# Kernel optimization log

Measured on AMD Instinct MI355X. Metric: run time of the kernel, lower is better.

The kernel has to match this reference:

```python
import jax, jax.numpy as jnp
import numpy as np

N_HEAD = 16
TOPK = 2


def _forward(x, noise, Wk, Wv, Wq, Wo, Wg, Wn):
    B, T, C = x.shape
    E = Wg.shape[1]
    H = N_HEAD
    D = C // H
    x2 = x.reshape(-1, C)  # [N, C], N = B*T
    # noisy gating: logits + randn * softplus(noise_proj)
    gate_logits = x2 @ Wg + noise * jax.nn.softplus(x2 @ Wn)  # [N, E]
    w, sel = jax.lax.top_k(gate_logits, TOPK)                 # [N, K]
    w = jax.nn.softmax(w.astype(jnp.float32), axis=1).astype(x.dtype)
    # shared keys/values across experts
    k = (x @ Wk).reshape(B, T, H, D)
    v = (x @ Wv).reshape(B, T, H, D)
    # per-expert queries for all tokens, gathered per selected expert below
    q_all = jnp.einsum('btc,eco->bteo', x, Wq)  # [B, T, E, C]
    causal = jnp.tril(jnp.ones((T, T), dtype=bool))  # key j visible to query t iff j <= t
    scale = 1.0 / np.sqrt(D).astype(np.float32)
    sel_bt = sel.reshape(B, T, TOPK)
    w_bt = w.reshape(B, T, TOPK)
    out = jnp.zeros_like(x)
    for s in range(TOPK):  # small fixed loop over top-k slots
        e = sel_bt[:, :, s]  # [B, T] expert id per token
        q = jnp.take_along_axis(q_all, e[:, :, None, None], axis=2)[:, :, 0, :]  # [B, T, C]
        qh = q.reshape(B, T, H, D)
        scores = jnp.einsum('bthd,bjhd->bhtj', qh, k) * scale  # [B, H, T, T]
        scores = jnp.where(causal[None, None], scores, -jnp.inf)
        p = jax.nn.softmax(scores, axis=-1)
        attn = jnp.einsum('bhtj,bjhd->bthd', p, v).reshape(B, T, C)
        o_all = jnp.einsum('btc,eco->bteo', attn, Wo)  # [B, T, E, C]
        o = jnp.take_along_axis(o_all, e[:, :, None, None], axis=2)[:, :, 0, :]
        out = out + w_bt[:, :, s:s + 1] * o
    return out


def setup_inputs() -> dict:
    key = jax.random.key(0)
    ks = jax.random.split(key, 8)
    B, T, C, E = 4, 1024, 1024, 8
    s = 0.02
    x = jax.random.normal(ks[0], (B, T, C), jnp.float32)
    noise = jax.random.normal(ks[1], (B * T, E), jnp.float32)
    Wk = jax.random.normal(ks[2], (C, C), jnp.float32) * s
    Wv = jax.random.normal(ks[3], (C, C), jnp.float32) * s
    Wq = jax.random.normal(ks[4], (E, C, C), jnp.float32) * s
    Wo = jax.random.normal(ks[5], (E, C, C), jnp.float32) * s
    Wg = jax.random.normal(ks[6], (C, E), jnp.float32) * s
    Wn = jax.random.normal(ks[7], (C, E), jnp.float32) * s
    return {'x': x, 'noise': noise, 'Wk': Wk, 'Wv': Wv, 'Wq': Wq, 'Wo': Wo, 'Wg': Wg, 'Wn': Wn}


def reference(x, noise, Wk, Wv, Wq, Wo, Wg, Wn):
    return _forward(x, noise, Wk, Wv, Wq, Wo, Wg, Wn)
```

## Files before the change

kernel.cpp:

```cpp
#include <hip/hip_runtime.h>
#include <hip/hip_bf16.h>

#define TSEQ   1024
#define NC     1024
#define MBT    4096
#define NEXP   8
#define NHEAD  16
#define DHEAD  64
#define PERM_CAP 10240
#define MAXTILES 96

typedef __attribute__((ext_vector_type(8))) short bf16x8;
typedef __attribute__((ext_vector_type(4))) float f32x4;

static __device__ __forceinline__ unsigned short f2bf(float x){
    union { __hip_bfloat16 h; unsigned short u; } v;
    v.h = __float2bfloat16(x);
    return v.u;
}

__global__ __launch_bounds__(64)
void gate_kernel(const float* __restrict__ x, const float* __restrict__ noise,
                 const float* __restrict__ Wg, const float* __restrict__ Wn,
                 int* __restrict__ epair, float* __restrict__ wpair){
    int t = blockIdx.x;
    int lane = threadIdx.x;
    float ag[8] = {0,0,0,0,0,0,0,0};
    float an[8] = {0,0,0,0,0,0,0,0};
    const float* xr = x + (size_t)t * NC;
    for (int c = lane; c < NC; c += 64){
        float xv = xr[c];
        #pragma unroll
        for (int j = 0; j < 8; j++){
            ag[j] = fmaf(xv, Wg[c*8 + j], ag[j]);
            an[j] = fmaf(xv, Wn[c*8 + j], an[j]);
        }
    }
    #pragma unroll
    for (int j = 0; j < 8; j++){
        #pragma unroll
        for (int o = 32; o >= 1; o >>= 1){
            ag[j] += __shfl_xor(ag[j], o, 64);
            an[j] += __shfl_xor(an[j], o, 64);
        }
    }
    if (lane == 0){
        float lg[8];
        #pragma unroll
        for (int j = 0; j < 8; j++){
            float z = an[j];
            float sp = (z > 20.f) ? z : log1pf(expf(z));
            lg[j] = ag[j] + noise[(size_t)t*8 + j] * sp;
        }
        int i0 = 0; float v0 = lg[0];
        #pragma unroll
        for (int j = 1; j < 8; j++) if (lg[j] > v0){ v0 = lg[j]; i0 = j; }
        int i1 = -1; float v1 = -3.4e38f;
        #pragma unroll
        for (int j = 0; j < 8; j++) if (j != i0 && lg[j] > v1){ v1 = lg[j]; i1 = j; }
        float e1 = expf(v1 - v0);
        float w0 = 1.f / (1.f + e1);
        epair[2*t]   = i0;
        epair[2*t+1] = i1;
        wpair[2*t]   = w0;
        wpair[2*t+1] = e1 * w0;
    }
}

__global__ void transpose_cvt(const float* __restrict__ W, unsigned short* __restrict__ Wt){
    __shared__ float t[32][33];
    size_t base = (size_t)blockIdx.z * NC * NC;
    int k0 = blockIdx.x * 32, n0 = blockIdx.y * 32;
    int tx = threadIdx.x, ty = threadIdx.y;
    #pragma unroll
    for (int i = 0; i < 4; i++)
        t[ty + i*8][tx] = W[base + (size_t)(k0 + ty + i*8)*NC + n0 + tx];
    __syncthreads();
    #pragma unroll
    for (int i = 0; i < 4; i++)
        Wt[base + (size_t)(n0 + ty + i*8)*NC + k0 + tx] = f2bf(t[tx][ty + i*8]);
}

__global__ void cvt_x(const float* __restrict__ x, unsigned short* __restrict__ xb){
    int idx = blockIdx.x * blockDim.x + threadIdx.x;
    float4 v = ((const float4*)x)[idx];
    ushort4 o;
    o.x = f2bf(v.x); o.y = f2bf(v.y); o.z = f2bf(v.z); o.w = f2bf(v.w);
    ((ushort4*)xb)[idx] = o;
}

__global__ void transpose_v(const unsigned short* __restrict__ kvb, unsigned short* __restrict__ vbT){
    __shared__ unsigned short sh[32][33];
    int b = blockIdx.z;
    int c0 = blockIdx.x * 32, t0 = blockIdx.y * 32;
    int tx = threadIdx.x, ty = threadIdx.y;
    #pragma unroll
    for (int i = 0; i < 4; i++)
        sh[ty + i*8][tx] = kvb[((size_t)(b*TSEQ + t0 + ty + i*8))*2048 + 1024 + c0 + tx];
    __syncthreads();
    #pragma unroll
    for (int i = 0; i < 4; i++){
        int c = c0 + ty + i*8;
        vbT[((size_t)(b*NC + c))*TSEQ + t0 + tx] = sh[tx][ty + i*8];
    }
}

__global__ void group_build(const int* __restrict__ epair, int* __restrict__ cursor,
                            int* __restrict__ tile_g, int* __restrict__ tile_pos,
                            int* __restrict__ ntiles, int* __restrict__ perm){
    __shared__ int cnt[16];
    int tid = threadIdx.x;
    if (tid < 16) cnt[tid] = 0;
    __syncthreads();
    for (int p = tid; p < 2*MBT; p += 256){
        int g = ((p & 1) << 3) | epair[p];
        atomicAdd(&cnt[g], 1);
    }
    for (int i = tid; i < PERM_CAP; i += 256) perm[i] = -1;
    __syncthreads();
    if (tid == 0){
        int off = 0, tt = 0;
        for (int g = 0; g < 16; g++){
            int c = cnt[g];
            cursor[g] = off;
            int nt = (c + 127) >> 7;
            for (int i = 0; i < nt; i++){ tile_g[tt] = g; tile_pos[tt] = off + i*128; tt++; }
            off += nt << 7;
        }
        ntiles[0] = tt;
    }
}

__global__ void fill_perm(const int* __restrict__ epair, int* __restrict__ cursor,
                          int* __restrict__ perm){
    int p = blockIdx.x * blockDim.x + threadIdx.x;
    if (p < 2*MBT){
        int g = ((p & 1) << 3) | epair[p];
        int pos = atomicAdd(&cursor[g], 1);
        perm[pos] = p;
    }
}

template<int MODE>
__global__ __launch_bounds__(256)
void gemm_k(const unsigned short* __restrict__ A,
            const unsigned short* __restrict__ Bt,
            void* __restrict__ Cout,
            const int* __restrict__ perm,
            const int* __restrict__ tile_g,
            const int* __restrict__ tile_pos,
            const int* __restrict__ ntiles,
            const float* __restrict__ wpair,
            int nout){
    int ntile = blockIdx.x;
    int slot  = blockIdx.y;
    int tpos = 0;
    const unsigned short* bt = Bt;
    if (MODE != 0){
        if (slot >= ntiles[0]) return;
        int g = tile_g[slot];
        bt = Bt + (size_t)(g & 7) * NC * NC;
        tpos = tile_pos[slot];
    }
    __shared__ __align__(16) unsigned short As[128][72];
    __shared__ __align__(16) unsigned short Bs[128][72];
    int tid = threadIdx.x;
    int lane = tid & 63, wv = tid >> 6;
    int wr = wv >> 1, wc = wv & 1;
    int quad = lane >> 4, l15 = lane & 15;

    int r0 = tid >> 3;
    int c8 = (tid & 7) * 8;
    const unsigned short* ap[4];
    const unsigned short* bp[4];
    #pragma unroll
    for (int i = 0; i < 4; i++){
        int row = r0 + i*32;
        if (MODE == 0){
            ap[i] = A + (size_t)(slot*128 + row) * NC + c8;
        } else {
            int p = perm[tpos + row];
            if (p >= 0){
                if (MODE == 1) ap[i] = A + (size_t)(p >> 1) * NC + c8;
                else           ap[i] = A + (size_t)(p & 1) * MBT * NC + (size_t)(p >> 1) * NC + c8;
            } else ap[i] = nullptr;
        }
        bp[i] = bt + (size_t)(ntile*128 + row) * NC + c8;
    }

    f32x4 acc[4][4];
    #pragma unroll
    for (int i = 0; i < 4; i++)
        #pragma unroll
        for (int j = 0; j < 4; j++) acc[i][j] = (f32x4){0.f,0.f,0.f,0.f};

    for (int kk = 0; kk < NC; kk += 64){
        #pragma unroll
        for (int i = 0; i < 4; i++){
            int row = r0 + i*32;
            uint4 av = ap[i] ? *(const uint4*)(ap[i] + kk) : make_uint4(0,0,0,0);
            uint4 bv = *(const uint4*)(bp[i] + kk);
            *(uint4*)&As[row][c8] = av;
            *(uint4*)&Bs[row][c8] = bv;
        }
        __syncthreads();
        #pragma unroll
        for (int kh = 0; kh < 2; kh++){
            bf16x8 af[4], bfr[4];
            #pragma unroll
            for (int mi = 0; mi < 4; mi++) af[mi]  = *(const bf16x8*)&As[wr*64 + mi*16 + l15][kh*32 + quad*8];
            #pragma unroll
            for (int ni = 0; ni < 4; ni++) bfr[ni] = *(const bf16x8*)&Bs[wc*64 + ni*16 + l15][kh*32 + quad*8];
            #pragma unroll
            for (int mi = 0; mi < 4; mi++)
                #pragma unroll
                for (int ni = 0; ni < 4; ni++)
                    acc[mi][ni] = __builtin_amdgcn_mfma_f32_16x16x32_bf16(af[mi], bfr[ni], acc[mi][ni], 0, 0, 0);
        }
        __syncthreads();
    }

    int colbase = ntile*128 + wc*64 + l15;
    #pragma unroll
    for (int mi = 0; mi < 4; mi++){
        #pragma unroll
        for (int r = 0; r < 4; r++){
            int m = wr*64 + mi*16 + quad*4 + r;
            if (MODE == 0){
                unsigned short* co = (unsigned short*)Cout + (size_t)(slot*128 + m) * nout + colbase;
                #pragma unroll
                for (int ni = 0; ni < 4; ni++) co[ni*16] = f2bf(acc[mi][ni][r]);
            } else {
                int p = perm[tpos + m];
                if (p >= 0){
                    if (MODE == 1){
                        unsigned short* co = (unsigned short*)Cout + (size_t)p * NC + colbase;
                        #pragma unroll
                        for (int ni = 0; ni < 4; ni++) co[ni*16] = f2bf(0.125f * acc[mi][ni][r]);
                    } else {
                        float w = wpair[p];
                        float* co = (float*)Cout + (size_t)(p & 1) * MBT * NC + (size_t)(p >> 1) * NC + colbase;
                        #pragma unroll
                        for (int ni = 0; ni < 4; ni++) co[ni*16] = w * acc[mi][ni][r];
                    }
                }
            }
        }
    }
}

__global__ void combine(const float* __restrict__ os, float* __restrict__ out){
    size_t i = ((size_t)blockIdx.x * 256 + threadIdx.x) * 4;
    float4 a = *(const float4*)(os + i);
    float4 b = *(const float4*)(os + (size_t)MBT*NC + i);
    float4 r; r.x = a.x+b.x; r.y = a.y+b.y; r.z = a.z+b.z; r.w = a.w+b.w;
    *(float4*)(out + i) = r;
}

__global__ __launch_bounds__(256)
void attn_k(const unsigned short* __restrict__ qsel, const unsigned short* __restrict__ kvb,
            const unsigned short* __restrict__ vbT, unsigned short* __restrict__ attnb){
    int b = blockIdx.y >> 4, h = blockIdx.y & 15;
    int s = blockIdx.z;
    int tid = threadIdx.x, lane = tid & 63, wv = tid >> 6;
    int quad = lane >> 4, l15 = lane & 15;

    __shared__ __align__(16) unsigned short ksh[64][72];
    __shared__ __align__(16) unsigned short vsh[64][72];
    __shared__ __align__(16) unsigned short pwork[4][32][72];

    #pragma unroll
    for (int half = 0; half < 2; half++){
        int qb = half ? (7 - blockIdx.x) : blockIdx.x;
        int qbase = qb*128 + wv*32;
        int ig[2] = { qbase + l15, qbase + 16 + l15 };

        bf16x8 qf[2][2];
        #pragma unroll
        for (int isub = 0; isub < 2; isub++){
            const unsigned short* qrow = qsel + (((size_t)(b*TSEQ + qbase + isub*16 + l15))*2 + s)*NC + h*DHEAD;
            qf[isub][0] = *(const bf16x8*)(qrow + quad*8);
            qf[isub][1] = *(const bf16x8*)(qrow + 32 + quad*8);
        }

        float mrun[2] = {-1e30f, -1e30f}, lrun[2] = {0.f, 0.f};
        f32x4 oacc[4][2];
        #pragma unroll
        for (int d = 0; d < 4; d++)
            #pragma unroll
            for (int i = 0; i < 2; i++) oacc[d][i] = (f32x4){0.f,0.f,0.f,0.f};

        int njt = qb*2 + 2;
        for (int jt = 0; jt < njt; jt++){
            #pragma unroll
            for (int it = 0; it < 2; it++){
                int idx = it*256 + tid;
                int r = idx >> 3, cc = (idx & 7) * 8;
                *(uint4*)&ksh[r][cc] = *(const uint4*)(kvb + ((size_t)(b*TSEQ + jt*64 + r))*2048 + h*DHEAD + cc);
                *(uint4*)&vsh[r][cc] = *(const uint4*)(vbT + ((size_t)(b*NC + h*DHEAD + r))*TSEQ + jt*64 + cc);
            }
            __syncthreads();

            if (jt*64 <= qbase + 31){
                f32x4 sac[4][2];
                #pragma unroll
                for (int jsub = 0; jsub < 4; jsub++){
                    bf16x8 kf0 = *(const bf16x8*)&ksh[jsub*16 + l15][quad*8];
                    bf16x8 kf1 = *(const bf16x8*)&ksh[jsub*16 + l15][32 + quad*8];
                    #pragma unroll
                    for (int isub = 0; isub < 2; isub++){
                        f32x4 z = (f32x4){0.f,0.f,0.f,0.f};
                        z = __builtin_amdgcn_mfma_f32_16x16x32_bf16(kf0, qf[isub][0], z, 0, 0, 0);
                        z = __builtin_amdgcn_mfma_f32_16x16x32_bf16(kf1, qf[isub][1], z, 0, 0, 0);
                        sac[jsub][isub] = z;
                    }
                }
                bool need_mask = (jt*64 + 63 > qbase);
                float sv[2][16];
                #pragma unroll
                for (int jsub = 0; jsub < 4; jsub++){
                    #pragma unroll
                    for (int r = 0; r < 4; r++){
                        int j = jt*64 + jsub*16 + quad*4 + r;
                        #pragma unroll
                        for (int isub = 0; isub < 2; isub++){
                            float v = sac[jsub][isub][r];
                            if (need_mask && j > ig[isub]) v = -1e30f;
                            sv[isub][jsub*4 + r] = v;
                        }
                    }
                }
                #pragma unroll
                for (int isub = 0; isub < 2; isub++){
                    float tm = sv[isub][0];
                    #pragma unroll
                    for (int k = 1; k < 16; k++) tm = fmaxf(tm, sv[isub][k]);
                    tm = fmaxf(tm, __shfl_xor(tm, 16, 64));
                    tm = fmaxf(tm, __shfl_xor(tm, 32, 64));
                    float mn = fmaxf(mrun[isub], tm);
                    float alpha = __expf(mrun[isub] - mn);
                    float rs = 0.f;
                    #pragma unroll
                    for (int k = 0; k < 16; k++){
                        float p = __expf(sv[isub][k] - mn);
                        sv[isub][k] = p; rs += p;
                    }
                    rs += __shfl_xor(rs, 16, 64);
                    rs += __shfl_xor(rs, 32, 64);
                    lrun[isub] = lrun[isub]*alpha + rs; mrun[isub] = mn;
                    #pragma unroll
                    for (int d = 0; d < 4; d++) oacc[d][isub] = oacc[d][isub] * alpha;
                    #pragma unroll
                    for (int jsub = 0; jsub < 4; jsub++){
                        ushort4 pk;
                        pk.x = f2bf(sv[isub][jsub*4 + 0]);
                        pk.y = f2bf(sv[isub][jsub*4 + 1]);
                        pk.z = f2bf(sv[isub][jsub*4 + 2]);
                        pk.w = f2bf(sv[isub][jsub*4 + 3]);
                        *(ushort4*)&pwork[wv][isub*16 + l15][jsub*16 + quad*4] = pk;
                    }
                }
                bf16x8 pf[2][2];
                #pragma unroll
                for (int kh = 0; kh < 2; kh++)
                    #pragma unroll
                    for (int isub = 0; isub < 2; isub++)
                        pf[kh][isub] = *(const bf16x8*)&pwork[wv][isub*16 + l15][kh*32 + quad*8];
                #pragma unroll
                for (int dsub = 0; dsub < 4; dsub++){
                    bf16x8 vf0 = *(const bf16x8*)&vsh[dsub*16 + l15][quad*8];
                    bf16x8 vf1 = *(const bf16x8*)&vsh[dsub*16 + l15][32 + quad*8];
                    #pragma unroll
                    for (int isub = 0; isub < 2; isub++){
                        oacc[dsub][isub] = __builtin_amdgcn_mfma_f32_16x16x32_bf16(vf0, pf[0][isub], oacc[dsub][isub], 0, 0, 0);
                        oacc[dsub][isub] = __builtin_amdgcn_mfma_f32_16x16x32_bf16(vf1, pf[1][isub], oacc[dsub][isub], 0, 0, 0);
                    }
                }
            }
            __syncthreads();
        }

        float inv[2] = { 1.f / lrun[0], 1.f / lrun[1] };
        #pragma unroll
        for (int dsub = 0; dsub < 4; dsub++)
            #pragma unroll
            for (int isub = 0; isub < 2; isub++){
                ushort4 ok;
                ok.x = f2bf(oacc[dsub][isub][0] * inv[isub]);
                ok.y = f2bf(oacc[dsub][isub][1] * inv[isub]);
                ok.z = f2bf(oacc[dsub][isub][2] * inv[isub]);
                ok.w = f2bf(oacc[dsub][isub][3] * inv[isub]);
                *(ushort4*)&pwork[wv][isub*16 + l15][dsub*16 + quad*4] = ok;
            }
        #pragma unroll
        for (int rr = 0; rr < 4; rr++){
            int idx = rr*64 + lane;
            int il = idx >> 3, cc = (idx & 7) * 8;
            int t = qb*128 + wv*32 + il;
            *(uint4*)(attnb + (size_t)s*MBT*NC + ((size_t)(b*TSEQ + t))*NC + h*DHEAD + cc) =
                *(const uint4*)&pwork[wv][il][cc];
        }
    }
}

extern "C" void kernel_launch(void* const* d_in, const int* in_sizes, int n_in,
                              void* d_out, int out_size, void* d_ws, size_t ws_size,
                              hipStream_t stream){
    (void)in_sizes; (void)n_in; (void)out_size; (void)ws_size;
    const float* x     = (const float*)d_in[0];
    const float* noise = (const float*)d_in[1];
    const float* Wk    = (const float*)d_in[2];
    const float* Wv    = (const float*)d_in[3];
    const float* Wq    = (const float*)d_in[4];
    const float* Wo    = (const float*)d_in[5];
    const float* Wg    = (const float*)d_in[6];
    const float* Wn    = (const float*)d_in[7];
    float* out = (float*)d_out;

    char* ws = (char*)d_ws;
    size_t off = 0;
    auto alloc = [&](size_t bytes) -> void* {
        void* p = ws + off;
        off += (bytes + 255) & ~(size_t)255;
        return p;
    };
    unsigned short* xb    = (unsigned short*)alloc((size_t)MBT*NC*2);
    unsigned short* vbufT = (unsigned short*)alloc((size_t)MBT*NC*2);
    unsigned short* kvbuf = (unsigned short*)alloc((size_t)MBT*2048*2);
    unsigned short* qselb = (unsigned short*)alloc((size_t)MBT*2*NC*2);
    unsigned short* attnb = (unsigned short*)alloc((size_t)2*MBT*NC*2);
    unsigned short* Wkvt  = (unsigned short*)alloc((size_t)2*NC*NC*2);
    unsigned short* Wqt   = (unsigned short*)alloc((size_t)NEXP*NC*NC*2);
    unsigned short* Wot   = (unsigned short*)alloc((size_t)NEXP*NC*NC*2);
    int*   epair   = (int*)alloc(2*MBT*4);
    float* wpair   = (float*)alloc(2*MBT*4);
    int*   perm    = (int*)alloc(PERM_CAP*4);
    int*   cursor  = (int*)alloc(16*4);
    int*   tile_g  = (int*)alloc(MAXTILES*4);
    int*   tile_pos= (int*)alloc(MAXTILES*4);
    int*   ntiles  = (int*)alloc(4);

    float* osbuf = (float*)kvbuf;

    transpose_cvt<<<dim3(32,32,1), dim3(32,8), 0, stream>>>(Wk, Wkvt);
    transpose_cvt<<<dim3(32,32,1), dim3(32,8), 0, stream>>>(Wv, Wkvt + (size_t)NC*NC);
    transpose_cvt<<<dim3(32,32,8), dim3(32,8), 0, stream>>>(Wq, Wqt);
    transpose_cvt<<<dim3(32,32,8), dim3(32,8), 0, stream>>>(Wo, Wot);
    cvt_x<<<4096, 256, 0, stream>>>(x, xb);
    gate_kernel<<<4096, 64, 0, stream>>>(x, noise, Wg, Wn, epair, wpair);
    group_build<<<1, 256, 0, stream>>>(epair, cursor, tile_g, tile_pos, ntiles, perm);
    fill_perm<<<32, 256, 0, stream>>>(epair, cursor, perm);

    gemm_k<0><<<dim3(16,32), 256, 0, stream>>>(xb, Wkvt, kvbuf, nullptr, nullptr, nullptr, nullptr, nullptr, 2048);
    transpose_v<<<dim3(32,32,4), dim3(32,8), 0, stream>>>(kvbuf, vbufT);
    gemm_k<1><<<dim3(8,MAXTILES), 256, 0, stream>>>(xb, Wqt, qselb, perm, tile_g, tile_pos, ntiles, nullptr, NC);

    attn_k<<<dim3(4,64,2), 256, 0, stream>>>(qselb, kvbuf, vbufT, attnb);

    gemm_k<2><<<dim3(8,MAXTILES), 256, 0, stream>>>(attnb, Wot, osbuf, perm, tile_g, tile_pos, ntiles, wpair, NC);
    combine<<<4096, 256, 0, stream>>>(osbuf, out);
}
```

Baseline: 389.7 us.

## Use direct global-to-LDS loads with XOR-swizzled tiles in GEMM and attention

Replaces register-staged global loads plus LDS stores with 16-byte global_load_lds builtins in both the grouped GEMM and the attention kernel. The LDS tiles drop their padding, so an XOR swizzle on the 16-byte chunk index keeps fragment reads bank-conflict free. This is meant to remove VGPR staging and the extra LDS store instructions. Invalid permutation rows now load row 0 instead of zeros, which relies on the epilogue discarding those rows.

```diff
diff --git a/kernel.cpp b/kernel.cpp
--- a/kernel.cpp
+++ b/kernel.cpp
@@ -12,6 +12,13 @@
 
 typedef __attribute__((ext_vector_type(8))) short bf16x8;
 typedef __attribute__((ext_vector_type(4))) float f32x4;
+
+typedef __attribute__((address_space(3))) unsigned char* lds_ptr_t;
+typedef const __attribute__((address_space(1))) unsigned char* glb_ptr_t;
+
+static __device__ __forceinline__ void gload16(const void* g, void* l){
+    __builtin_amdgcn_global_load_lds((glb_ptr_t)g, (lds_ptr_t)l, 16, 0, 0);
+}
 
 static __device__ __forceinline__ unsigned short f2bf(float x){
     union { __hip_bfloat16 h; unsigned short u; } v;
@@ -162,30 +169,30 @@
         bt = Bt + (size_t)(g & 7) * NC * NC;
         tpos = tile_pos[slot];
     }
-    __shared__ __align__(16) unsigned short As[128][72];
-    __shared__ __align__(16) unsigned short Bs[128][72];
+    __shared__ __align__(16) unsigned short As[128*64];
+    __shared__ __align__(16) unsigned short Bs[128*64];
     int tid = threadIdx.x;
     int lane = tid & 63, wv = tid >> 6;
     int wr = wv >> 1, wc = wv & 1;
     int quad = lane >> 4, l15 = lane & 15;
 
-    int r0 = tid >> 3;
-    int c8 = (tid & 7) * 8;
-    const unsigned short* ap[4];
-    const unsigned short* bp[4];
-    #pragma unroll
-    for (int i = 0; i < 4; i++){
-        int row = r0 + i*32;
+    int laneR = lane >> 3;
+    int swz = ((lane & 7) ^ (laneR & 7)) * 8;
+
+    const unsigned short* ag[4];
+    const unsigned short* bg[4];
+    #pragma unroll
+    for (int it = 0; it < 4; it++){
+        int row = wv*32 + it*8 + laneR;
         if (MODE == 0){
-            ap[i] = A + (size_t)(slot*128 + row) * NC + c8;
+            ag[it] = A + (size_t)(slot*128 + row) * NC + swz;
         } else {
             int p = perm[tpos + row];
-            if (p >= 0){
-                if (MODE == 1) ap[i] = A + (size_t)(p >> 1) * NC + c8;
-                else           ap[i] = A + (size_t)(p & 1) * MBT * NC + (size_t)(p >> 1) * NC + c8;
-            } else ap[i] = nullptr;
-        }
-        bp[i] = bt + (size_t)(ntile*128 + row) * NC + c8;
+            if (p < 0) p = 0;
+            if (MODE == 1) ag[it] = A + (size_t)(p >> 1) * NC + swz;
+            else           ag[it] = A + (size_t)(p & 1) * MBT * NC + (size_t)(p >> 1) * NC + swz;
+        }
+        bg[it] = bt + (size_t)(ntile*128 + row) * NC + swz;
     }
 
     f32x4 acc[4][4];
@@ -196,21 +203,20 @@
 
     for (int kk = 0; kk < NC; kk += 64){
         #pragma unroll
-        for (int i = 0; i < 4; i++){
-            int row = r0 + i*32;
-            uint4 av = ap[i] ? *(const uint4*)(ap[i] + kk) : make_uint4(0,0,0,0);
-            uint4 bv = *(const uint4*)(bp[i] + kk);
-            *(uint4*)&As[row][c8] = av;
-            *(uint4*)&Bs[row][c8] = bv;
+        for (int it = 0; it < 4; it++){
+            gload16(ag[it] + kk, &As[(wv*32 + it*8)*64]);
+            gload16(bg[it] + kk, &Bs[(wv*32 + it*8)*64]);
         }
         __syncthreads();
         #pragma unroll
         for (int kh = 0; kh < 2; kh++){
             bf16x8 af[4], bfr[4];
             #pragma unroll
-            for (int mi = 0; mi < 4; mi++) af[mi]  = *(const bf16x8*)&As[wr*64 + mi*16 + l15][kh*32 + quad*8];
-            #pragma unroll
-            for (int ni = 0; ni < 4; ni++) bfr[ni] = *(const bf16x8*)&Bs[wc*64 + ni*16 + l15][kh*32 + quad*8];
+            for (int mi = 0; mi < 4; mi++)
+                af[mi]  = *(const bf16x8*)&As[(wr*64 + mi*16 + l15)*64 + (((kh*4 + quad) ^ (l15 & 7))*8)];
+            #pragma unroll
+            for (int ni = 0; ni < 4; ni++)
+                bfr[ni] = *(const bf16x8*)&Bs[(wc*64 + ni*16 + l15)*64 + (((kh*4 + quad) ^ (l15 & 7))*8)];
             #pragma unroll
             for (int mi = 0; mi < 4; mi++)
                 #pragma unroll
@@ -264,9 +270,11 @@
     int s = blockIdx.z;
     int tid = threadIdx.x, lane = tid & 63, wv = tid >> 6;
     int quad = lane >> 4, l15 = lane & 15;
-
-    __shared__ __align__(16) unsigned short ksh[64][72];
-    __shared__ __align__(16) unsigned short vsh[64][72];
+    int laneR = lane >> 3;
+    int swz = ((lane & 7) ^ (laneR & 7)) * 8;
+
+    __shared__ __align__(16) unsigned short ksh[64*64];
+    __shared__ __align__(16) unsigned short vsh[64*64];
     __shared__ __align__(16) unsigned short pwork[4][32][72];
 
     #pragma unroll
@@ -294,10 +302,11 @@
         for (int jt = 0; jt < njt; jt++){
             #pragma unroll
             for (int it = 0; it < 2; it++){
-                int idx = it*256 + tid;
-                int r = idx >> 3, cc = (idx & 7) * 8;
-                *(uint4*)&ksh[r][cc] = *(const uint4*)(kvb + ((size_t)(b*TSEQ + jt*64 + r))*2048 + h*DHEAD + cc);
-                *(uint4*)&vsh[r][cc] = *(const uint4*)(vbT + ((size_t)(b*NC + h*DHEAD + r))*TSEQ + jt*64 + cc);
+                int r = wv*16 + it*8 + laneR;
+                gload16(kvb + ((size_t)(b*TSEQ + jt*64 + r))*2048 + h*DHEAD + swz,
+                        &ksh[(wv*16 + it*8)*64]);
+                gload16(vbT + ((size_t)(b*NC + h*DHEAD + r))*TSEQ + jt*64 + swz,
+                        &vsh[(wv*16 + it*8)*64]);
             }
             __syncthreads();
 
@@ -305,8 +314,8 @@
                 f32x4 sac[4][2];
                 #pragma unroll
                 for (int jsub = 0; jsub < 4; jsub++){
-                    bf16x8 kf0 = *(const bf16x8*)&ksh[jsub*16 + l15][quad*8];
-                    bf16x8 kf1 = *(const bf16x8*)&ksh[jsub*16 + l15][32 + quad*8];
+                    bf16x8 kf0 = *(const bf16x8*)&ksh[(jsub*16 + l15)*64 + ((quad     ^ (l15 & 7))*8)];
+                    bf16x8 kf1 = *(const bf16x8*)&ksh[(jsub*16 + l15)*64 + (((4+quad) ^ (l15 & 7))*8)];
                     #pragma unroll
                     for (int isub = 0; isub < 2; isub++){
                         f32x4 z = (f32x4){0.f,0.f,0.f,0.f};
@@ -368,8 +377,8 @@
                         pf[kh][isub] = *(const bf16x8*)&pwork[wv][isub*16 + l15][kh*32 + quad*8];
                 #pragma unroll
                 for (int dsub = 0; dsub < 4; dsub++){
-                    bf16x8 vf0 = *(const bf16x8*)&vsh[dsub*16 + l15][quad*8];
-                    bf16x8 vf1 = *(const bf16x8*)&vsh[dsub*16 + l15][32 + quad*8];
+                    bf16x8 vf0 = *(const bf16x8*)&vsh[(dsub*16 + l15)*64 + ((quad     ^ (l15 & 7))*8)];
+                    bf16x8 vf1 = *(const bf16x8*)&vsh[(dsub*16 + l15)*64 + (((4+quad) ^ (l15 & 7))*8)];
                     #pragma unroll
                     for (int isub = 0; isub < 2; isub++){
                         oacc[dsub][isub] = __builtin_amdgcn_mfma_f32_16x16x32_bf16(vf0, pf[0][isub], oacc[dsub][isub], 0, 0, 0);
```

Measured after the change: 372.4 us. -4.4%, faster.
